# Optimization experiments

Hardware: AMD Instinct MI355X
Metric: run time of the kernel (lower is better)

Reference implementation:

```python
import jax, jax.numpy as jnp
import numpy as np

B, S, D = 4, 16, 512          # batch, seq, attention_dim
V, T = 32000, 18              # vocab_size, tree_depth
INNER = V - 1                 # internal nodes of Huffman tree


def setup_inputs() -> dict:
    key = jax.random.key(0)
    k_att, k_w, k_idx, k_bit = jax.random.split(key, 4)
    att = jax.random.normal(k_att, (B, S, D), dtype=jnp.float32)
    weight = jax.random.normal(k_w, (INNER, D), dtype=jnp.float32) * 0.02
    path_index = jax.random.randint(k_idx, (V * T,), 0, INNER, dtype=jnp.int64)
    # left/right branch bits: sign=+1,bias=0 -> p ; sign=-1,bias=1 -> 1-p
    bits = jax.random.randint(k_bit, (V * T,), 0, 2).astype(jnp.float32)
    path_sign = 1.0 - 2.0 * bits
    path_bias = bits
    return {
        "att": att,
        "weight": weight,
        "path_index": path_index,
        "path_sign": path_sign,
        "path_bias": path_bias,
        "vocab_size": V,
        "tree_depth": T,
    }


def reference(att, weight, path_index, path_sign, path_bias, vocab_size, tree_depth):
    # h: sigmoid of linear projection onto internal-node vectors  [B,S,INNER]
    h = jax.nn.sigmoid(jnp.einsum("bsd,nd->bsn", att, weight))
    # gather per-(token,depth) internal-node probs, flip via sign/bias
    g = jnp.take(h, path_index, axis=-1) * path_sign + path_bias  # [B,S,V*T]
    Hm = g.reshape(att.shape[0], -1, vocab_size, tree_depth)      # [B,S,V,T]
    return jnp.sum(jnp.log(Hm), axis=-1)                          # [B,S,V]
```

## Files before the change

kernel.cpp:

```cpp
#include <hip/hip_runtime.h>
#include <hip/hip_bf16.h>

#define BS    64
#define DDIM  512
#define NV    32000
#define TD    18
#define INNER 31999
#define NPAD  32000

typedef __attribute__((ext_vector_type(8))) short short8;
typedef __attribute__((ext_vector_type(4))) float floatx4;

__device__ __forceinline__ float bf16_to_f32(unsigned short u) {
    union { unsigned int i; float f; } v; v.i = ((unsigned int)u) << 16; return v.f;
}
__device__ __forceinline__ unsigned short f32_to_bf16(float f) {
    union { float f; unsigned int i; } v; v.f = f;
    unsigned int r = v.i + 0x7FFFu + ((v.i >> 16) & 1u);
    return (unsigned short)(r >> 16);
}
__device__ __forceinline__ short8 cvt8(const float* p) {
    float4 a = *(const float4*)p;
    float4 b = *(const float4*)(p + 4);
    short8 f;
    f[0] = (short)f32_to_bf16(a.x); f[1] = (short)f32_to_bf16(a.y);
    f[2] = (short)f32_to_bf16(a.z); f[3] = (short)f32_to_bf16(a.w);
    f[4] = (short)f32_to_bf16(b.x); f[5] = (short)f32_to_bf16(b.y);
    f[6] = (short)f32_to_bf16(b.z); f[7] = (short)f32_to_bf16(b.w);
    return f;
}

__global__ __launch_bounds__(256) void gemm_logsig(
    const float* __restrict__ att,
    const float* __restrict__ weight,
    unsigned int* __restrict__ pairsT)
{
    const int lane = threadIdx.x & 63;
    const int wave = threadIdx.x >> 6;
    const int nb   = blockIdx.x * 64 + wave * 16;
    const int l15  = lane & 15;
    const int quad = lane >> 4;

    floatx4 acc[4];
#pragma unroll
    for (int i = 0; i < 4; ++i) acc[i] = (floatx4){0.f, 0.f, 0.f, 0.f};

    int brow = nb + l15;
    if (brow > INNER - 1) brow = INNER - 1;
    const float* bbase = weight + (size_t)brow * DDIM + quad * 8;
    const float* abase = att + l15 * DDIM + quad * 8;

#pragma unroll 4
    for (int k0 = 0; k0 < DDIM; k0 += 32) {
        short8 bfrag = cvt8(bbase + k0);
#pragma unroll
        for (int mt = 0; mt < 4; ++mt) {
            short8 afrag = cvt8(abase + mt * 16 * DDIM + k0);
            acc[mt] = __builtin_amdgcn_mfma_f32_16x16x32_bf16(afrag, bfrag, acc[mt], 0, 0, 0);
        }
    }

    const int n = nb + l15;
    if (n < INNER) {
        unsigned int* dst = pairsT + (size_t)n * 64 + quad * 4;
#pragma unroll
        for (int mt = 0; mt < 4; ++mt) {
            uint4 pk;
#pragma unroll
            for (int r = 0; r < 4; ++r) {
                float x = acc[mt][r];
                float lp = -(fmaxf(-x, 0.f) + __logf(1.f + __expf(-fabsf(x))));
                float lm = lp - x;
                ((unsigned int*)&pk)[r] = (unsigned int)f32_to_bf16(lp)
                                        | ((unsigned int)f32_to_bf16(lm) << 16);
            }
            *(uint4*)(dst + mt * 16) = pk;
        }
    }
}

__global__ __launch_bounds__(256) void gather_T(
    const unsigned int* __restrict__ pairsT,
    const int* __restrict__ idx,
    const unsigned int* __restrict__ signbits,
    float* __restrict__ out)
{
    const int lane = threadIdx.x & 63;
    const int wave = threadIdx.x >> 6;

    const unsigned int* w = (const unsigned int*)idx;
    unsigned int orw = 0;
#pragma unroll
    for (int j = 1; j < 16; j += 2) orw |= w[j];
    const bool i64 = (orw == 0u);

#pragma unroll
    for (int g = 0; g < 4; ++g) {
        const int v0 = blockIdx.x * 64 + wave * 16 + g * 4;
        const int i0 = v0 * TD;
        float a0 = 0.f, a1 = 0.f, a2 = 0.f, a3 = 0.f;
#pragma unroll
        for (int t = 0; t < TD; ++t) {
            int j0 = i0 + t, j1 = i0 + TD + t, j2 = i0 + 2 * TD + t, j3 = i0 + 3 * TD + t;
            unsigned int n0 = __builtin_amdgcn_readfirstlane(i64 ? idx[2 * j0] : idx[j0]);
            unsigned int n1 = __builtin_amdgcn_readfirstlane(i64 ? idx[2 * j1] : idx[j1]);
            unsigned int n2 = __builtin_amdgcn_readfirstlane(i64 ? idx[2 * j2] : idx[j2]);
            unsigned int n3 = __builtin_amdgcn_readfirstlane(i64 ? idx[2 * j3] : idx[j3]);
            unsigned int s0 = __builtin_amdgcn_readfirstlane(signbits[j0]) >> 31;
            unsigned int s1 = __builtin_amdgcn_readfirstlane(signbits[j1]) >> 31;
            unsigned int s2 = __builtin_amdgcn_readfirstlane(signbits[j2]) >> 31;
            unsigned int s3 = __builtin_amdgcn_readfirstlane(signbits[j3]) >> 31;
            unsigned int p0 = pairsT[(size_t)n0 * 64 + lane];
            unsigned int p1 = pairsT[(size_t)n1 * 64 + lane];
            unsigned int p2 = pairsT[(size_t)n2 * 64 + lane];
            unsigned int p3 = pairsT[(size_t)n3 * 64 + lane];
            a0 += bf16_to_f32(s0 ? (unsigned short)(p0 >> 16) : (unsigned short)(p0 & 0xFFFFu));
            a1 += bf16_to_f32(s1 ? (unsigned short)(p1 >> 16) : (unsigned short)(p1 & 0xFFFFu));
            a2 += bf16_to_f32(s2 ? (unsigned short)(p2 >> 16) : (unsigned short)(p2 & 0xFFFFu));
            a3 += bf16_to_f32(s3 ? (unsigned short)(p3 >> 16) : (unsigned short)(p3 & 0xFFFFu));
        }
        float4 st = {a0, a1, a2, a3};
        *(float4*)(out + (size_t)lane * NV + v0) = st;
    }
}

extern "C" void kernel_launch(void* const* d_in, const int* in_sizes, int n_in,
                              void* d_out, int out_size, void* d_ws, size_t ws_size,
                              hipStream_t stream)
{
    const float*        att    = (const float*)d_in[0];
    const float*        weight = (const float*)d_in[1];
    const int*          pidx   = (const int*)d_in[2];
    const unsigned int* psign  = (const unsigned int*)d_in[3];
    float* out = (float*)d_out;

    unsigned int* pairsT = (unsigned int*)d_ws;

    gemm_logsig<<<500, 256, 0, stream>>>(att, weight, pairsT);
    gather_T<<<500, 256, 0, stream>>>(pairsT, pidx, psign, out);
}
```

Before: 164.9 us.

## Pre-convert att to bf16 and split GEMM K across two wave groups

Adds a small kernel that converts att to bf16 once, so the GEMM no longer reconverts each A fragment in every block. The GEMM block doubles to 512 threads, with two wave groups each covering half of K. The partial accumulators are then combined through shared memory before the log-sigmoid epilogue. This raises the number of waves in flight and shortens each wave's K loop, at the cost of an extra launch, a barrier and LDS traffic.

New measurement: 152.7 us. 7.4% less time.

```diff
diff --git a/kernel.cpp b/kernel.cpp
--- a/kernel.cpp
+++ b/kernel.cpp
@@ -19,27 +19,32 @@
     unsigned int r = v.i + 0x7FFFu + ((v.i >> 16) & 1u);
     return (unsigned short)(r >> 16);
 }
-__device__ __forceinline__ short8 cvt8(const float* p) {
-    float4 a = *(const float4*)p;
-    float4 b = *(const float4*)(p + 4);
-    short8 f;
-    f[0] = (short)f32_to_bf16(a.x); f[1] = (short)f32_to_bf16(a.y);
-    f[2] = (short)f32_to_bf16(a.z); f[3] = (short)f32_to_bf16(a.w);
-    f[4] = (short)f32_to_bf16(b.x); f[5] = (short)f32_to_bf16(b.y);
-    f[6] = (short)f32_to_bf16(b.z); f[7] = (short)f32_to_bf16(b.w);
-    return f;
+
+__global__ __launch_bounds__(256) void cvt_att(
+    const float4* __restrict__ att, ushort4* __restrict__ attb)
+{
+    int i = blockIdx.x * 256 + threadIdx.x;
+    float4 a = att[i];
+    ushort4 r;
+    r.x = f32_to_bf16(a.x); r.y = f32_to_bf16(a.y);
+    r.z = f32_to_bf16(a.z); r.w = f32_to_bf16(a.w);
+    attb[i] = r;
 }
 
-__global__ __launch_bounds__(256) void gemm_logsig(
-    const float* __restrict__ att,
+__global__ __launch_bounds__(512, 4) void gemm_logsig(
+    const unsigned short* __restrict__ attb,
     const float* __restrict__ weight,
     unsigned int* __restrict__ pairsT)
 {
-    const int lane = threadIdx.x & 63;
-    const int wave = threadIdx.x >> 6;
-    const int nb   = blockIdx.x * 64 + wave * 16;
-    const int l15  = lane & 15;
-    const int quad = lane >> 4;
+    __shared__ floatx4 cmb[4][64][4];
+    const int tid   = threadIdx.x;
+    const int wave  = tid >> 6;
+    const int lane  = tid & 63;
+    const int ntile = wave & 3;
+    const int khalf = wave >> 2;
+    const int nb    = blockIdx.x * 64 + ntile * 16;
+    const int l15   = lane & 15;
+    const int quad  = lane >> 4;
 
     floatx4 acc[4];
 #pragma unroll
@@ -47,34 +52,50 @@
 
     int brow = nb + l15;
     if (brow > INNER - 1) brow = INNER - 1;
-    const float* bbase = weight + (size_t)brow * DDIM + quad * 8;
-    const float* abase = att + l15 * DDIM + quad * 8;
+    const float*          bbase = weight + (size_t)brow * DDIM + khalf * 256 + quad * 8;
+    const unsigned short* abase = attb + l15 * DDIM + khalf * 256 + quad * 8;
 
 #pragma unroll 4
-    for (int k0 = 0; k0 < DDIM; k0 += 32) {
-        short8 bfrag = cvt8(bbase + k0);
+    for (int k0 = 0; k0 < 256; k0 += 32) {
+        float4 b0 = *(const float4*)(bbase + k0);
+        float4 b1 = *(const float4*)(bbase + k0 + 4);
+        short8 bfrag;
+        bfrag[0] = (short)f32_to_bf16(b0.x); bfrag[1] = (short)f32_to_bf16(b0.y);
+        bfrag[2] = (short)f32_to_bf16(b0.z); bfrag[3] = (short)f32_to_bf16(b0.w);
+        bfrag[4] = (short)f32_to_bf16(b1.x); bfrag[5] = (short)f32_to_bf16(b1.y);
+        bfrag[6] = (short)f32_to_bf16(b1.z); bfrag[7] = (short)f32_to_bf16(b1.w);
 #pragma unroll
         for (int mt = 0; mt < 4; ++mt) {
-            short8 afrag = cvt8(abase + mt * 16 * DDIM + k0);
+            short8 afrag = *(const short8*)(abase + mt * 16 * DDIM + k0);
             acc[mt] = __builtin_amdgcn_mfma_f32_16x16x32_bf16(afrag, bfrag, acc[mt], 0, 0, 0);
         }
     }
 
-    const int n = nb + l15;
-    if (n < INNER) {
-        unsigned int* dst = pairsT + (size_t)n * 64 + quad * 4;
+    if (khalf == 1) {
 #pragma unroll
-        for (int mt = 0; mt < 4; ++mt) {
-            uint4 pk;
+        for (int mt = 0; mt < 4; ++mt) cmb[ntile][lane][mt] = acc[mt];
+    }
+    __syncthreads();
+    if (khalf == 0) {
 #pragma unroll
-            for (int r = 0; r < 4; ++r) {
-                float x = acc[mt][r];
-                float lp = -(fmaxf(-x, 0.f) + __logf(1.f + __expf(-fabsf(x))));
-                float lm = lp - x;
-                ((unsigned int*)&pk)[r] = (unsigned int)f32_to_bf16(lp)
-                                        | ((unsigned int)f32_to_bf16(lm) << 16);
+        for (int mt = 0; mt < 4; ++mt) acc[mt] += cmb[ntile][lane][mt];
+
+        const int n = nb + l15;
+        if (n < INNER) {
+            unsigned int* dst = pairsT + (size_t)n * 64 + quad * 4;
+#pragma unroll
+            for (int mt = 0; mt < 4; ++mt) {
+                uint4 pk;
+#pragma unroll
+                for (int r = 0; r < 4; ++r) {
+                    float x = acc[mt][r];
+                    float lp = -(fmaxf(-x, 0.f) + __logf(1.f + __expf(-fabsf(x))));
+                    float lm = lp - x;
+                    ((unsigned int*)&pk)[r] = (unsigned int)f32_to_bf16(lp)
+                                            | ((unsigned int)f32_to_bf16(lm) << 16);
+                }
+                *(uint4*)(dst + mt * 16) = pk;
             }
-            *(uint4*)(dst + mt * 16) = pk;
         }
     }
 }
@@ -134,8 +155,11 @@
     const unsigned int* psign  = (const unsigned int*)d_in[3];
     float* out = (float*)d_out;
 
-    unsigned int* pairsT = (unsigned int*)d_ws;
+    char* ws = (char*)d_ws;
+    unsigned int*   pairsT = (unsigned int*)ws;
+    unsigned short* attb   = (unsigned short*)(ws + 8192000);
 
-    gemm_logsig<<<500, 256, 0, stream>>>(att, weight, pairsT);
+    cvt_att<<<32, 256, 0, stream>>>((const float4*)att, (ushort4*)attb);
+    gemm_logsig<<<500, 512, 0, stream>>>(attb, weight, pairsT);
     gather_T<<<500, 256, 0, stream>>>(pairsT, pidx, psign, out);
 }
```
